# Kernel tuning notes

Hardware: AMD Instinct MI355X
Metric: run time of the kernel (lower is better)

## Reference

```python
import jax, jax.numpy as jnp
import numpy as np

# Gate hyperparameters (from init_kwargs)
DIM = 4096
N_EXPERTS = 256        # n_routed_experts
N_GROUPS = 8           # n_expert_groups
TOPK_GROUPS = 4        # n_limited_groups
TOPK = 8               # n_activated_experts
ROUTE_SCALE = 1.0
N_TOKENS = 16384       # batch * seq_len flattened


def setup_inputs() -> dict:
    key = jax.random.key(0)
    kx, kw = jax.random.split(key)
    x = jax.random.normal(kx, (N_TOKENS, DIM), dtype=jnp.float32)
    # xavier-ish scale for the gate projection weight [n_experts, dim]
    weight = jax.random.normal(kw, (N_EXPERTS, DIM), dtype=jnp.float32) * (1.0 / np.sqrt(DIM))
    return {"x": x, "weight": weight}


def reference(x, weight):
    T = x.shape[0]
    # scores = linear(x, weight)  -> [T, E]
    logits = jnp.einsum('td,ed->te', x, weight)
    # score_func == 'softmax' computed in fp32 (torch: softmax(dim=-1, dtype=float32))
    scores = jax.nn.softmax(logits.astype(jnp.float32), axis=-1)
    original_scores = scores

    # group-limited routing (n_groups > 1, no bias -> amax per group)
    sg = scores.reshape(T, N_GROUPS, N_EXPERTS // N_GROUPS)   # [T, G, E/G]
    group_scores = jnp.max(sg, axis=-1)                        # [T, G]
    _, gidx = jax.lax.top_k(group_scores, TOPK_GROUPS)         # [T, topk_groups]
    keep = jnp.zeros((T, N_GROUPS), dtype=bool)
    keep = keep.at[jnp.arange(T)[:, None], gidx].set(True)
    masked = jnp.where(keep[:, :, None], sg, -jnp.inf).reshape(T, N_EXPERTS)

    # top-k expert selection; weights gathered from the un-masked scores
    _, idx = jax.lax.top_k(masked, TOPK)                       # [T, topk]
    weights = jnp.take_along_axis(original_scores, idx, axis=1)
    weights = weights * ROUTE_SCALE
    return weights.astype(x.dtype), idx
```

## Files before the change

### kernel.cpp

```cpp
#include <hip/hip_runtime.h>
#include <math.h>
#include <stdint.h>

#define NTOK   16384
#define DIM    4096
#define NEXP   256
#define TOPKG  4
#define TOPK   8
#define NSPLIT 4
#define KCHUNK (DIM / NSPLIT)
#define BM     128
#define BK     32

typedef float v4f   __attribute__((ext_vector_type(4)));
typedef short short8 __attribute__((ext_vector_type(8)));

__device__ inline unsigned short f2bf(float x) {
    unsigned u = __float_as_uint(x);
    return (unsigned short)((u + 0x7fffu + ((u >> 16) & 1u)) >> 16);
}
__device__ inline float bf2f(unsigned short h) {
    return __uint_as_float(((unsigned)h) << 16);
}

__global__ __launch_bounds__(256) void wprep(const float* __restrict__ W,
                                             unsigned short* __restrict__ Wh,
                                             unsigned short* __restrict__ Wl) {
    int i = (blockIdx.x * 256 + threadIdx.x) * 4;
    float4 v = *(const float4*)(W + i);
    ushort4 h, l;
    h.x = f2bf(v.x); l.x = f2bf(v.x - bf2f(h.x));
    h.y = f2bf(v.y); l.y = f2bf(v.y - bf2f(h.y));
    h.z = f2bf(v.z); l.z = f2bf(v.z - bf2f(h.z));
    h.w = f2bf(v.w); l.w = f2bf(v.w - bf2f(h.w));
    *(ushort4*)(Wh + i) = h;
    *(ushort4*)(Wl + i) = l;
}

__global__ __launch_bounds__(256, 2) void gate_gemm(const float* __restrict__ X,
                                                    const unsigned short* __restrict__ Wh,
                                                    const unsigned short* __restrict__ Wl,
                                                    float* __restrict__ P) {
    __shared__ __align__(16) unsigned short Ah[BM * BK];
    __shared__ __align__(16) unsigned short Al[BM * BK];
    __shared__ __align__(16) unsigned short Bh[NEXP * BK];
    __shared__ __align__(16) unsigned short Bl[NEXP * BK];

    const int t  = threadIdx.x;
    const int bm = blockIdx.x * BM;
    const int z  = blockIdx.y;
    const int k0 = z * KCHUNK;

    const int l  = t & 63;
    const int w  = t >> 6;
    const int lm = l & 15;
    const int lq = l >> 4;

    const int ar = t >> 1;
    const int ak = (t & 1) * 16;
    const float* xrow = X + (size_t)(bm + ar) * DIM + k0 + ak;

    v4f acc[8][4] = {};

    for (int kr = 0; kr < KCHUNK; kr += BK) {
        __syncthreads();

#pragma unroll
        for (int i = 0; i < 4; ++i) {
            int flat = i * 256 + t;
            int e = flat >> 2, q = flat & 3;
            const unsigned short* gh = Wh + (size_t)e * DIM + k0 + kr + q * 8;
            const unsigned short* gl = Wl + (size_t)e * DIM + k0 + kr + q * 8;
            __builtin_amdgcn_global_load_lds(
                (const __attribute__((address_space(1))) unsigned int*)gh,
                (__attribute__((address_space(3))) unsigned int*)&Bh[flat * 8], 16, 0, 0);
            __builtin_amdgcn_global_load_lds(
                (const __attribute__((address_space(1))) unsigned int*)gl,
                (__attribute__((address_space(3))) unsigned int*)&Bl[flat * 8], 16, 0, 0);
        }

        float4 xv[4];
#pragma unroll
        for (int i = 0; i < 4; ++i) xv[i] = *(const float4*)(xrow + kr + i * 4);
#pragma unroll
        for (int i = 0; i < 4; ++i) {
            ushort4 h, lo;
            h.x = f2bf(xv[i].x); lo.x = f2bf(xv[i].x - bf2f(h.x));
            h.y = f2bf(xv[i].y); lo.y = f2bf(xv[i].y - bf2f(h.y));
            h.z = f2bf(xv[i].z); lo.z = f2bf(xv[i].z - bf2f(h.z));
            h.w = f2bf(xv[i].w); lo.w = f2bf(xv[i].w - bf2f(h.w));
            *(ushort4*)&Ah[ar * BK + ak + i * 4] = h;
            *(ushort4*)&Al[ar * BK + ak + i * 4] = lo;
        }

        __syncthreads();

        short8 bh[4], bl[4];
#pragma unroll
        for (int c = 0; c < 4; ++c) {
            int e = w * 64 + c * 16 + lm;
            bh[c] = *(const short8*)&Bh[e * BK + lq * 8];
            bl[c] = *(const short8*)&Bl[e * BK + lq * 8];
        }
#pragma unroll
        for (int r = 0; r < 8; ++r) {
            int m = r * 16 + lm;
            short8 ah = *(const short8*)&Ah[m * BK + lq * 8];
            short8 al = *(const short8*)&Al[m * BK + lq * 8];
#pragma unroll
            for (int c = 0; c < 4; ++c) {
                acc[r][c] = __builtin_amdgcn_mfma_f32_16x16x32_bf16(ah, bh[c], acc[r][c], 0, 0, 0);
                acc[r][c] = __builtin_amdgcn_mfma_f32_16x16x32_bf16(ah, bl[c], acc[r][c], 0, 0, 0);
                acc[r][c] = __builtin_amdgcn_mfma_f32_16x16x32_bf16(al, bh[c], acc[r][c], 0, 0, 0);
            }
        }
    }

    float* Pb = P + ((size_t)z * NTOK + bm) * NEXP;
#pragma unroll
    for (int r = 0; r < 8; ++r)
#pragma unroll
        for (int c = 0; c < 4; ++c)
#pragma unroll
            for (int g = 0; g < 4; ++g)
                Pb[(size_t)(r * 16 + lq * 4 + g) * NEXP + w * 64 + c * 16 + lm] = acc[r][c][g];
}

__global__ __launch_bounds__(256) void gate_route(const float* __restrict__ P,
                                                  float* __restrict__ outw,
                                                  float* __restrict__ outi) {
    const int lane = threadIdx.x & 63;
    const int tok  = (blockIdx.x * blockDim.x + threadIdx.x) >> 6;
    if (tok >= NTOK) return;

    float l[4] = {0.f, 0.f, 0.f, 0.f};
#pragma unroll
    for (int z = 0; z < NSPLIT; ++z) {
        float4 v = *(const float4*)(P + ((size_t)z * NTOK + tok) * NEXP + lane * 4);
        l[0] += v.x; l[1] += v.y; l[2] += v.z; l[3] += v.w;
    }

    float lmax = fmaxf(fmaxf(l[0], l[1]), fmaxf(l[2], l[3]));
    float m = lmax;
#pragma unroll
    for (int o = 32; o; o >>= 1) m = fmaxf(m, __shfl_xor(m, o));

    float s = __expf(l[0] - m) + __expf(l[1] - m) + __expf(l[2] - m) + __expf(l[3] - m);
#pragma unroll
    for (int o = 32; o; o >>= 1) s += __shfl_xor(s, o);

    float gm = lmax;
#pragma unroll
    for (int o = 4; o; o >>= 1) gm = fmaxf(gm, __shfl_xor(gm, o));

    const int g = lane >> 3;
    int rank = 0;
#pragma unroll
    for (int gg = 0; gg < 8; ++gg) {
        float vg = __shfl(gm, gg * 8);
        rank += (vg > gm) || (vg == gm && gg < g);
    }
    const bool allowed = rank < TOPKG;

    float mv[4];
#pragma unroll
    for (int j = 0; j < 4; ++j) mv[j] = allowed ? l[j] : -INFINITY;

    float wsel = 0.0f;
    int   isel = 0;

    for (int k = 0; k < TOPK; ++k) {
        float bv = mv[0];
        int   bi = lane * 4;
        if (mv[1] > bv) { bv = mv[1]; bi = lane * 4 + 1; }
        if (mv[2] > bv) { bv = mv[2]; bi = lane * 4 + 2; }
        if (mv[3] > bv) { bv = mv[3]; bi = lane * 4 + 3; }
#pragma unroll
        for (int o = 32; o; o >>= 1) {
            float ov = __shfl_xor(bv, o);
            int   oi = __shfl_xor(bi, o);
            if (ov > bv || (ov == bv && oi < bi)) { bv = ov; bi = oi; }
        }
        if (lane == k) { wsel = __expf(bv - m) / s; isel = bi; }
        if ((bi >> 2) == lane) mv[bi & 3] = -INFINITY;
    }

    if (lane < TOPK) {
        outw[(size_t)tok * TOPK + lane] = wsel;
        outi[(size_t)tok * TOPK + lane] = (float)isel;
    }
}

extern "C" void kernel_launch(void* const* d_in, const int* in_sizes, int n_in,
                              void* d_out, int out_size, void* d_ws, size_t ws_size,
                              hipStream_t stream) {
    const float* x  = (const float*)d_in[0];
    const float* wt = (const float*)d_in[1];

    float* P = (float*)d_ws;
    unsigned short* Wh = (unsigned short*)((char*)d_ws + (size_t)NSPLIT * NTOK * NEXP * 4);
    unsigned short* Wl = Wh + (size_t)NEXP * DIM;

    float* outw = (float*)d_out;
    float* outi = (float*)d_out + (size_t)NTOK * TOPK;

    wprep<<<(NEXP * DIM) / (256 * 4), 256, 0, stream>>>(wt, Wh, Wl);

    dim3 ggrid(NTOK / BM, NSPLIT);
    gate_gemm<<<ggrid, 256, 0, stream>>>(x, Wh, Wl, P);

    gate_route<<<(NTOK * 64) / 256, 256, 0, stream>>>(P, outw, outi);
}
```

Measured before the change: 433.5 us.

## Enlarge GEMM tile to 256 rows with 2x2 wave layout and register prefetch of X

Doubles the token tile to 256 rows and arranges the four waves as a 2x2 grid, each computing a 128x128 output block with 8x8 accumulators, so each loaded W tile is reused across twice as many tokens. X rows are now loaded one per thread and prefetched into registers for the next K step while the MFMAs run, and the A tile in LDS is padded to a stride of 34 to reduce bank conflicts. The cost is much higher register pressure (256 accumulator floats per thread, occupancy bound dropped to 1 block), and the grid is halved to 256 blocks, which may leave compute units underused. The per-thread stores of 32 contiguous floats also change the global load coalescing pattern for X.

```diff
diff --git a/kernel.cpp b/kernel.cpp
--- a/kernel.cpp
+++ b/kernel.cpp
@@ -9,10 +9,11 @@
 #define TOPK   8
 #define NSPLIT 4
 #define KCHUNK (DIM / NSPLIT)
-#define BM     128
+#define BM     256
 #define BK     32
-
-typedef float v4f   __attribute__((ext_vector_type(4)));
+#define ALD    34
+
+typedef float v4f    __attribute__((ext_vector_type(4)));
 typedef short short8 __attribute__((ext_vector_type(8)));
 
 __device__ inline unsigned short f2bf(float x) {
@@ -37,12 +38,12 @@
     *(ushort4*)(Wl + i) = l;
 }
 
-__global__ __launch_bounds__(256, 2) void gate_gemm(const float* __restrict__ X,
+__global__ __launch_bounds__(256, 1) void gate_gemm(const float* __restrict__ X,
                                                     const unsigned short* __restrict__ Wh,
                                                     const unsigned short* __restrict__ Wl,
                                                     float* __restrict__ P) {
-    __shared__ __align__(16) unsigned short Ah[BM * BK];
-    __shared__ __align__(16) unsigned short Al[BM * BK];
+    __shared__ __align__(16) unsigned short Ah[BM * ALD];
+    __shared__ __align__(16) unsigned short Al[BM * ALD];
     __shared__ __align__(16) unsigned short Bh[NEXP * BK];
     __shared__ __align__(16) unsigned short Bl[NEXP * BK];
 
@@ -53,14 +54,18 @@
 
     const int l  = t & 63;
     const int w  = t >> 6;
+    const int wr = w >> 1;
+    const int wc = w & 1;
     const int lm = l & 15;
     const int lq = l >> 4;
 
-    const int ar = t >> 1;
-    const int ak = (t & 1) * 16;
-    const float* xrow = X + (size_t)(bm + ar) * DIM + k0 + ak;
-
-    v4f acc[8][4] = {};
+    const float* xrow = X + (size_t)(bm + t) * DIM + k0;
+
+    float4 xv[8];
+#pragma unroll
+    for (int i = 0; i < 8; ++i) xv[i] = *(const float4*)(xrow + i * 4);
+
+    v4f acc[8][8] = {};
 
     for (int kr = 0; kr < KCHUNK; kr += BK) {
         __syncthreads();
@@ -68,9 +73,8 @@
 #pragma unroll
         for (int i = 0; i < 4; ++i) {
             int flat = i * 256 + t;
-            int e = flat >> 2, q = flat & 3;
-            const unsigned short* gh = Wh + (size_t)e * DIM + k0 + kr + q * 8;
-            const unsigned short* gl = Wl + (size_t)e * DIM + k0 + kr + q * 8;
+            const unsigned short* gh = Wh + (size_t)(flat >> 2) * DIM + k0 + kr + (flat & 3) * 8;
+            const unsigned short* gl = Wl + (size_t)(flat >> 2) * DIM + k0 + kr + (flat & 3) * 8;
             __builtin_amdgcn_global_load_lds(
                 (const __attribute__((address_space(1))) unsigned int*)gh,
                 (__attribute__((address_space(3))) unsigned int*)&Bh[flat * 8], 16, 0, 0);
@@ -79,36 +83,38 @@
                 (__attribute__((address_space(3))) unsigned int*)&Bl[flat * 8], 16, 0, 0);
         }
 
-        float4 xv[4];
-#pragma unroll
-        for (int i = 0; i < 4; ++i) xv[i] = *(const float4*)(xrow + kr + i * 4);
-#pragma unroll
-        for (int i = 0; i < 4; ++i) {
+#pragma unroll
+        for (int i = 0; i < 8; ++i) {
             ushort4 h, lo;
             h.x = f2bf(xv[i].x); lo.x = f2bf(xv[i].x - bf2f(h.x));
             h.y = f2bf(xv[i].y); lo.y = f2bf(xv[i].y - bf2f(h.y));
             h.z = f2bf(xv[i].z); lo.z = f2bf(xv[i].z - bf2f(h.z));
             h.w = f2bf(xv[i].w); lo.w = f2bf(xv[i].w - bf2f(h.w));
-            *(ushort4*)&Ah[ar * BK + ak + i * 4] = h;
-            *(ushort4*)&Al[ar * BK + ak + i * 4] = lo;
+            *(ushort4*)&Ah[t * ALD + i * 4] = h;
+            *(ushort4*)&Al[t * ALD + i * 4] = lo;
         }
 
         __syncthreads();
 
-        short8 bh[4], bl[4];
-#pragma unroll
-        for (int c = 0; c < 4; ++c) {
-            int e = w * 64 + c * 16 + lm;
+        if (kr + BK < KCHUNK) {
+#pragma unroll
+            for (int i = 0; i < 8; ++i) xv[i] = *(const float4*)(xrow + kr + BK + i * 4);
+        }
+
+        short8 bh[8], bl[8];
+#pragma unroll
+        for (int c = 0; c < 8; ++c) {
+            int e = wc * 128 + c * 16 + lm;
             bh[c] = *(const short8*)&Bh[e * BK + lq * 8];
             bl[c] = *(const short8*)&Bl[e * BK + lq * 8];
         }
 #pragma unroll
         for (int r = 0; r < 8; ++r) {
-            int m = r * 16 + lm;
-            short8 ah = *(const short8*)&Ah[m * BK + lq * 8];
-            short8 al = *(const short8*)&Al[m * BK + lq * 8];
-#pragma unroll
-            for (int c = 0; c < 4; ++c) {
+            int m = wr * 128 + r * 16 + lm;
+            short8 ah = *(const short8*)&Ah[m * ALD + lq * 8];
+            short8 al = *(const short8*)&Al[m * ALD + lq * 8];
+#pragma unroll
+            for (int c = 0; c < 8; ++c) {
                 acc[r][c] = __builtin_amdgcn_mfma_f32_16x16x32_bf16(ah, bh[c], acc[r][c], 0, 0, 0);
                 acc[r][c] = __builtin_amdgcn_mfma_f32_16x16x32_bf16(ah, bl[c], acc[r][c], 0, 0, 0);
                 acc[r][c] = __builtin_amdgcn_mfma_f32_16x16x32_bf16(al, bh[c], acc[r][c], 0, 0, 0);
@@ -120,10 +126,11 @@
 #pragma unroll
     for (int r = 0; r < 8; ++r)
 #pragma unroll
-        for (int c = 0; c < 4; ++c)
+        for (int c = 0; c < 8; ++c)
 #pragma unroll
             for (int g = 0; g < 4; ++g)
-                Pb[(size_t)(r * 16 + lq * 4 + g) * NEXP + w * 64 + c * 16 + lm] = acc[r][c][g];
+                Pb[(size_t)(wr * 128 + r * 16 + lq * 4 + g) * NEXP + wc * 128 + c * 16 + lm]
+                    = acc[r][c][g];
 }
 
 __global__ __launch_bounds__(256) void gate_route(const float* __restrict__ P,
```

Result: slower. 442.5 us (+2.1%).
